# Kernel optimization log

Hardware: AMD Instinct MI355X
Metric: run time of the kernel (lower is better)

Reference implementation:

```python
import jax, jax.numpy as jnp
import numpy as np

PI = 3.14159  # constant used in the torch module
N_QUBITS = 10
N_LAYERS = 4
B = 1024  # number of graphs


def _lin_init(k, fan_in, fan_out):
    k1, k2 = jax.random.split(k)
    s = 1.0 / np.sqrt(fan_in)
    W = jax.random.uniform(k1, (fan_in, fan_out), jnp.float32, -s, s)
    b = jax.random.uniform(k2, (fan_out,), jnp.float32, -s, s)
    return W, b


def setup_inputs():
    key = jax.random.key(0)
    ks = jax.random.split(key, 12)
    N, E, Fin, H, Emb = 32768, 131072, 128, 256, 128
    x = jax.random.normal(ks[0], (N, Fin), jnp.float32)
    edge_index = jax.random.randint(ks[1], (2, E), 0, N)
    batch = jnp.sort(jax.random.randint(ks[2], (N,), 0, B))
    edge_attr = jax.random.uniform(ks[3], (E, 4), dtype=jnp.float32)
    W1, b1 = _lin_init(ks[4], Fin, H)          # GCNConv 1
    W2, b2 = _lin_init(ks[5], H, Emb)          # GCNConv 2
    projW, projb = _lin_init(ks[6], Emb, N_QUBITS)
    vqc_weights = jax.random.uniform(ks[7], (N_LAYERS, N_QUBITS), jnp.float32, 0.0, 2 * np.pi)
    epW, epb = _lin_init(ks[8], 4, N_QUBITS - 1)
    cW1, cb1 = _lin_init(ks[9], Emb + N_QUBITS, 16)
    cW2, cb2 = _lin_init(ks[10], 16, 1)
    return dict(x=x, edge_index=edge_index, batch=batch, edge_attr=edge_attr,
                W1=W1, b1=b1, W2=W2, b2=b2, projW=projW, projb=projb,
                vqc_weights=vqc_weights, epW=epW, epb=epb,
                cW1=cW1, cb1=cb1, cW2=cW2, cb2=cb2)


def _gcn_conv(x, W, b, src, dst, n):
    # GCNConv with self-loops: sym-normalized aggregation of xW
    h = x @ W
    deg = jnp.zeros((n,), x.dtype).at[dst].add(1.0) + 1.0  # +1 self-loop
    dinv = jax.lax.rsqrt(deg)
    coef = (dinv[src] * dinv[dst])[:, None]
    agg = jnp.zeros_like(h).at[dst].add(h[src] * coef)
    return agg + h * (1.0 / deg)[:, None] + b


def _segment_mean(v, seg, n):
    tot = jnp.zeros((n, v.shape[1]), v.dtype).at[seg].add(v)
    cnt = jnp.zeros((n,), v.dtype).at[seg].add(1.0)
    return tot / jnp.clip(cnt, 1.0)[:, None]


def _run_vqc(q_in, weights, ep):
    # Batched real state-vector simulation. All gates (RY, CRY) are real.
    # Wire 0 = most significant bit (pennylane default.qubit convention).
    b = q_in.shape[0]
    dim = 2 ** N_QUBITS
    st = jnp.zeros((b, dim), q_in.dtype).at[:, 0].set(1.0)

    def ry(st, theta, w):
        th = jnp.broadcast_to(theta, (b,)) * 0.5
        c = jnp.cos(th)[:, None, None]
        s = jnp.sin(th)[:, None, None]
        r = st.reshape(b, 2 ** w, 2, -1)
        a0, a1 = r[:, :, 0], r[:, :, 1]
        return jnp.stack([c * a0 - s * a1, s * a0 + c * a1], axis=2).reshape(b, dim)

    def cry(st, theta, w):
        # control w, target w+1 (adjacent wires)
        th = jnp.broadcast_to(theta, (b,)) * 0.5
        c = jnp.cos(th)[:, None, None]
        s = jnp.sin(th)[:, None, None]
        r = st.reshape(b, 2 ** w, 2, 2, -1)
        a0, a1 = r[:, :, 1, 0], r[:, :, 1, 1]
        r = r.at[:, :, 1, 0].set(c * a0 - s * a1).at[:, :, 1, 1].set(s * a0 + c * a1)
        return r.reshape(b, dim)

    for i in range(N_QUBITS):                      # AngleEmbedding (RY)
        st = ry(st, q_in[:, i], i)
    for layer in range(N_LAYERS):
        for i in range(N_QUBITS):
            st = ry(st, weights[layer, i], i)
        for i in range(N_QUBITS - 1):
            st = cry(st, ep[:, i], i)

    probs = st * st
    zs = []
    for i in range(N_QUBITS):
        p = probs.reshape(b, 2 ** i, 2, -1).sum(axis=(1, 3))
        zs.append(p[:, 0] - p[:, 1])               # <PauliZ(i)>
    return jnp.stack(zs, axis=1)                   # [B, n_qubits]


def reference(x, edge_index, batch, edge_attr, W1, b1, W2, b2, projW, projb,
              vqc_weights, epW, epb, cW1, cb1, cW2, cb2):
    N = x.shape[0]
    src, dst = edge_index[0], edge_index[1]
    # GCN encoder: two GCNConv + ReLU, global mean pool (dropout = eval mode)
    h = jax.nn.relu(_gcn_conv(x, W1, b1, src, dst, N))
    h = jax.nn.relu(_gcn_conv(h, W2, b2, src, dst, N))
    emb = _segment_mean(h, batch, B)               # [B, gcn_embed]

    q_in = jnp.tanh(emb @ projW + projb) * PI      # [B, n_qubits]

    # scatter-mean edge pooling per graph, then edge projection
    edge_batch = batch[src]
    pooled_edge = _segment_mean(edge_attr, edge_batch, B)  # [B, 4]
    ep = pooled_edge @ epW + epb                   # [B, n_qubits-1]

    q_out = _run_vqc(q_in, vqc_weights, ep)        # [B, n_qubits]

    combined = jnp.concatenate([emb, q_out], axis=-1)
    hid = jax.nn.relu(combined @ cW1 + cb1)
    return hid @ cW2 + cb2                         # [B, num_tasks]
```

## Files before the change

### kernel.cpp

```cpp
#include <hip/hip_runtime.h>

#define PI_F 3.14159f
#define NQ 10

__global__ void k_zero(float4* __restrict__ p, int n4) {
  int i = blockIdx.x * blockDim.x + threadIdx.x;
  int stride = gridDim.x * blockDim.x;
  float4 z = {0.f, 0.f, 0.f, 0.f};
  for (; i < n4; i += stride) p[i] = z;
}

__global__ void k_edge_setup(const int* __restrict__ dstA, const int* __restrict__ srcA,
                             const float* __restrict__ eattr, int E,
                             int* __restrict__ cnt, float* __restrict__ nsum4,
                             float* __restrict__ necnt) {
  int e = blockIdx.x * blockDim.x + threadIdx.x;
  if (e >= E) return;
  atomicAdd(&cnt[dstA[e]], 1);
  int s = srcA[e];
  float4 v = *(const float4*)(eattr + (size_t)e * 4);
  atomicAdd(&nsum4[(size_t)s * 4 + 0], v.x);
  atomicAdd(&nsum4[(size_t)s * 4 + 1], v.y);
  atomicAdd(&nsum4[(size_t)s * 4 + 2], v.z);
  atomicAdd(&nsum4[(size_t)s * 4 + 3], v.w);
  atomicAdd(&necnt[s], 1.0f);
}

__global__ __launch_bounds__(1024) void k_scan1(const int* __restrict__ cnt,
                                                int* __restrict__ incl,
                                                int* __restrict__ bsum) {
  __shared__ int buf[1024];
  int t = threadIdx.x;
  int base = blockIdx.x << 10;
  buf[t] = cnt[base + t];
  __syncthreads();
#pragma unroll
  for (int off = 1; off < 1024; off <<= 1) {
    int x = (t >= off) ? buf[t - off] : 0;
    __syncthreads();
    buf[t] += x;
    __syncthreads();
  }
  incl[base + t] = buf[t];
  if (t == 1023) bsum[blockIdx.x] = buf[t];
}

__global__ void k_node_setup(const int* __restrict__ cnt, const int* __restrict__ incl,
                             const int* __restrict__ bsum, const int* __restrict__ batch,
                             int N, int Bn, int* __restrict__ rowStart,
                             int* __restrict__ pos, float* __restrict__ dinv,
                             float* __restrict__ invdeg, int* __restrict__ starts) {
  int i = blockIdx.x * blockDim.x + threadIdx.x;
  if (i >= N) return;
  int blk = i >> 10;
  int pre = 0;
  for (int j = 0; j < blk; j++) pre += bsum[j];
  int c = cnt[i];
  int inc = incl[i] + pre;
  rowStart[i + 1] = inc;
  pos[i] = inc - c;
  if (i == 0) rowStart[0] = 0;
  float d = (float)c + 1.0f;
  dinv[i] = 1.0f / sqrtf(d);
  invdeg[i] = 1.0f / d;
  int b = batch[i];
  int bp = (i == 0) ? -1 : batch[i - 1];
  for (int g = bp + 1; g <= b; g++) starts[g] = i;
  if (i == N - 1) {
    for (int g = b + 1; g <= Bn; g++) starts[g] = N;
  }
}

__global__ void k_fill(const int* __restrict__ dst, const int* __restrict__ srcA,
                       const float* __restrict__ dinv, int E, int* __restrict__ pos,
                       int* __restrict__ srcSorted, float* __restrict__ dcoef) {
  int e = blockIdx.x * blockDim.x + threadIdx.x;
  if (e >= E) return;
  int s = srcA[e];
  int slot = atomicAdd(&pos[dst[e]], 1);
  srcSorted[slot] = s;
  dcoef[slot] = dinv[s];
}

__global__ __launch_bounds__(256) void k_gemm(const float* __restrict__ A,
                                              const float* __restrict__ B,
                                              float* __restrict__ C,
                                              int M, int K, int N) {
  __shared__ float As[64][36];
  __shared__ float Bs[32][68];
  int t = threadIdx.x;
  int tx = t & 15, ty = t >> 4;
  int row0 = blockIdx.y * 64, col0 = blockIdx.x * 64;
  float acc[4][4] = {};
  for (int k0 = 0; k0 < K; k0 += 32) {
#pragma unroll
    for (int rep = 0; rep < 2; rep++) {
      int slot = t + rep * 256;
      int r = slot >> 3;
      int cg = (slot & 7) << 2;
      float4 v = *(const float4*)(A + (size_t)(row0 + r) * K + (k0 + cg));
      *(float4*)&As[r][cg] = v;
      int r2 = slot >> 4;
      int cg2 = (slot & 15) << 2;
      float4 w = *(const float4*)(B + (size_t)(k0 + r2) * N + (col0 + cg2));
      *(float4*)&Bs[r2][cg2] = w;
    }
    __syncthreads();
#pragma unroll
    for (int kk = 0; kk < 32; kk++) {
      float av[4];
      av[0] = As[ty * 4 + 0][kk];
      av[1] = As[ty * 4 + 1][kk];
      av[2] = As[ty * 4 + 2][kk];
      av[3] = As[ty * 4 + 3][kk];
      float4 b4 = *(const float4*)&Bs[kk][tx << 2];
      float bv[4] = {b4.x, b4.y, b4.z, b4.w};
#pragma unroll
      for (int i = 0; i < 4; i++)
#pragma unroll
        for (int j = 0; j < 4; j++) acc[i][j] = fmaf(av[i], bv[j], acc[i][j]);
    }
    __syncthreads();
  }
#pragma unroll
  for (int i = 0; i < 4; i++) {
    float4 v = {acc[i][0], acc[i][1], acc[i][2], acc[i][3]};
    *(float4*)(C + (size_t)(row0 + ty * 4 + i) * N + (col0 + (tx << 2))) = v;
  }
}

__global__ __launch_bounds__(256) void k_gcn_combine(
    const float* __restrict__ hlin, const int* __restrict__ srcSorted,
    const float* __restrict__ dcoef, const int* __restrict__ rowStart,
    const float* __restrict__ dinv, const float* __restrict__ invdeg,
    const float* __restrict__ bias, float* __restrict__ hout, int N, int C, int shift) {
  int gid = blockIdx.x * blockDim.x + threadIdx.x;
  int n = gid >> shift;
  if (n >= N) return;
  int cq = (gid & ((1 << shift) - 1)) << 2;
  int e0 = rowStart[n], e1 = rowStart[n + 1];
  float di = dinv[n];
  float ax = 0.f, ay = 0.f, az = 0.f, aw = 0.f;
  for (int e = e0; e < e1; e++) {
    int s = srcSorted[e];
    float coef = dcoef[e] * di;
    float4 v = *(const float4*)(hlin + (size_t)s * C + cq);
    ax = fmaf(coef, v.x, ax);
    ay = fmaf(coef, v.y, ay);
    az = fmaf(coef, v.z, az);
    aw = fmaf(coef, v.w, aw);
  }
  float idg = invdeg[n];
  float4 hv = *(const float4*)(hlin + (size_t)n * C + cq);
  float4 bv = *(const float4*)(bias + cq);
  float4 r;
  r.x = fmaxf(fmaf(hv.x, idg, ax) + bv.x, 0.f);
  r.y = fmaxf(fmaf(hv.y, idg, ay) + bv.y, 0.f);
  r.z = fmaxf(fmaf(hv.z, idg, az) + bv.z, 0.f);
  r.w = fmaxf(fmaf(hv.w, idg, aw) + bv.w, 0.f);
  *(float4*)(hout + (size_t)n * C + cq) = r;
}

__device__ __forceinline__ void apply_ry(float* st, int w, float c, float s, int t) {
  int str = 1 << (9 - w);
#pragma unroll
  for (int r = 0; r < 2; r++) {
    int p = t + 256 * r;
    int lo = p & (str - 1);
    int hi = p >> (9 - w);
    int a0 = (hi << (10 - w)) + lo;
    int a1 = a0 + str;
    float x0 = st[a0], x1 = st[a1];
    st[a0] = c * x0 - s * x1;
    st[a1] = s * x0 + c * x1;
  }
}

__device__ __forceinline__ void apply_cry(float* st, int w, float c, float s, int t) {
  int ts = 1 << (8 - w);
  int lo = t & (ts - 1);
  int hi = t >> (8 - w);
  int a0 = (hi << (10 - w)) + (ts << 1) + lo;
  int a1 = a0 + ts;
  float x0 = st[a0], x1 = st[a1];
  st[a0] = c * x0 - s * x1;
  st[a1] = s * x0 + c * x1;
}

__global__ __launch_bounds__(256) void k_vqc_head(
    const float* __restrict__ h2, const int* __restrict__ starts,
    const float* __restrict__ nsum4, const float* __restrict__ necnt,
    const float* __restrict__ projW, const float* __restrict__ projb,
    const float* __restrict__ vqcW, const float* __restrict__ epW,
    const float* __restrict__ epb, const float* __restrict__ cW1,
    const float* __restrict__ cb1, const float* __restrict__ cW2,
    const float* __restrict__ cb2, float* __restrict__ out) {
  int g = blockIdx.x;
  int t = threadIdx.x;
  __shared__ float st[1024];
  __shared__ float emb[128];
  __shared__ float csc[59], css[59];
  __shared__ float pool[5];
  __shared__ float zred[4][NQ];
  __shared__ float zq[NQ];
  __shared__ float hid[16];

  int s0 = starts[g], s1 = starts[g + 1];
  int cntn = s1 - s0;
  float invc = 1.0f / (float)(cntn > 0 ? cntn : 1);
  if (t < 128) {
    float sum = 0.f;
    for (int i = s0; i < s1; i++) sum += h2[(size_t)i * 128 + t];
    emb[t] = sum * invc;
  } else if (t >= 192) {
    int lane = t - 192;
    float p0 = 0.f, p1 = 0.f, p2 = 0.f, p3 = 0.f, pc = 0.f;
    for (int i = s0 + lane; i < s1; i += 64) {
      float4 v = *(const float4*)(nsum4 + (size_t)i * 4);
      p0 += v.x; p1 += v.y; p2 += v.z; p3 += v.w;
      pc += necnt[i];
    }
#pragma unroll
    for (int off = 32; off >= 1; off >>= 1) {
      p0 += __shfl_down(p0, off, 64);
      p1 += __shfl_down(p1, off, 64);
      p2 += __shfl_down(p2, off, 64);
      p3 += __shfl_down(p3, off, 64);
      pc += __shfl_down(pc, off, 64);
    }
    if (lane == 0) { pool[0] = p0; pool[1] = p1; pool[2] = p2; pool[3] = p3; pool[4] = pc; }
  }
  st[t] = 0.f; st[t + 256] = 0.f; st[t + 512] = 0.f; st[t + 768] = 0.f;
  __syncthreads();

  if (t < NQ) {
    float sum = projb[t];
    for (int k = 0; k < 128; k++) sum = fmaf(emb[k], projW[k * NQ + t], sum);
    float th = tanhf(sum) * PI_F * 0.5f;
    csc[t] = cosf(th);
    css[t] = sinf(th);
  } else if (t < NQ + 40) {
    float th = vqcW[t - NQ] * 0.5f;
    csc[t] = cosf(th);
    css[t] = sinf(th);
  } else if (t < 59) {
    int i = t - 50;
    float icnt = 1.0f / fmaxf(pool[4], 1.0f);
    float sum = epb[i];
    for (int j = 0; j < 4; j++) sum = fmaf(pool[j] * icnt, epW[j * 9 + i], sum);
    float th = sum * 0.5f;
    csc[t] = cosf(th);
    css[t] = sinf(th);
  }
  if (t == 0) st[0] = 1.0f;
  __syncthreads();

  for (int i = 0; i < NQ; i++) {
    apply_ry(st, i, csc[i], css[i], t);
    __syncthreads();
  }
  for (int L = 0; L < 4; L++) {
    for (int i = 0; i < NQ; i++) {
      apply_ry(st, i, csc[10 + L * 10 + i], css[10 + L * 10 + i], t);
      __syncthreads();
    }
    for (int i = 0; i < NQ - 1; i++) {
      apply_cry(st, i, csc[50 + i], css[50 + i], t);
      __syncthreads();
    }
  }

  float z[NQ];
#pragma unroll
  for (int i = 0; i < NQ; i++) z[i] = 0.f;
#pragma unroll
  for (int r = 0; r < 4; r++) {
    int a = t + 256 * r;
    float p = st[a] * st[a];
#pragma unroll
    for (int i = 0; i < NQ; i++) z[i] += ((a >> (9 - i)) & 1) ? -p : p;
  }
#pragma unroll
  for (int off = 32; off >= 1; off >>= 1) {
#pragma unroll
    for (int i = 0; i < NQ; i++) z[i] += __shfl_down(z[i], off, 64);
  }
  int wave = t >> 6, lane = t & 63;
  if (lane == 0) {
#pragma unroll
    for (int i = 0; i < NQ; i++) zred[wave][i] = z[i];
  }
  __syncthreads();
  if (t < NQ) zq[t] = zred[0][t] + zred[1][t] + zred[2][t] + zred[3][t];
  __syncthreads();

  if (t < 16) {
    float sum = cb1[t];
    for (int k = 0; k < 128; k++) sum = fmaf(emb[k], cW1[k * 16 + t], sum);
    for (int k = 0; k < NQ; k++) sum = fmaf(zq[k], cW1[(128 + k) * 16 + t], sum);
    hid[t] = fmaxf(sum, 0.f);
  }
  __syncthreads();
  if (t == 0) {
    float sum = cb2[0];
    for (int j = 0; j < 16; j++) sum = fmaf(hid[j], cW2[j], sum);
    out[g] = sum;
  }
}

extern "C" void kernel_launch(void* const* d_in, const int* in_sizes, int n_in,
                              void* d_out, int out_size, void* d_ws, size_t ws_size,
                              hipStream_t stream) {
  const float* x = (const float*)d_in[0];
  const int* ei = (const int*)d_in[1];
  const int* batch = (const int*)d_in[2];
  const float* eattr = (const float*)d_in[3];
  const float* W1 = (const float*)d_in[4];
  const float* b1 = (const float*)d_in[5];
  const float* W2 = (const float*)d_in[6];
  const float* b2 = (const float*)d_in[7];
  const float* projW = (const float*)d_in[8];
  const float* projb = (const float*)d_in[9];
  const float* vqcW = (const float*)d_in[10];
  const float* epW = (const float*)d_in[11];
  const float* epb = (const float*)d_in[12];
  const float* cW1 = (const float*)d_in[13];
  const float* cb1 = (const float*)d_in[14];
  const float* cW2 = (const float*)d_in[15];
  const float* cb2 = (const float*)d_in[16];
  float* out = (float*)d_out;

  const int N = in_sizes[0] / 128;
  const int E = in_sizes[1] / 2;
  const int Bn = out_size;

  const int* srcA = ei;
  const int* dstA = ei + E;

  char* ws = (char*)d_ws;
  float* bufA = (float*)ws;
  float* bufB = (float*)(ws + ((size_t)32 << 20));
  size_t off = (size_t)64 << 20;
  auto alloc = [&](size_t bytes) {
    size_t o = off;
    off += (bytes + 255) & ~(size_t)255;
    return o;
  };
  int* cnt = (int*)(ws + alloc((size_t)N * 4));
  float* nsum4 = (float*)(ws + alloc((size_t)N * 16));
  float* necnt = (float*)(ws + alloc((size_t)N * 4));
  size_t zeroEnd = off;
  int* rowStart = (int*)(ws + alloc((size_t)(N + 1) * 4));
  int* pos = (int*)(ws + alloc((size_t)N * 4));
  int* srcSorted = (int*)(ws + alloc((size_t)E * 4));
  float* dcoef = (float*)(ws + alloc((size_t)E * 4));
  float* dinv = (float*)(ws + alloc((size_t)N * 4));
  float* invdeg = (float*)(ws + alloc((size_t)N * 4));
  int* starts = (int*)(ws + alloc((size_t)(Bn + 1) * 4));
  int* incl = (int*)(ws + alloc((size_t)N * 4));
  int* bsum = (int*)(ws + alloc(64 * 4));

  int eblocks = (E + 255) / 256;
  int nblocks = (N + 255) / 256;
  int nb1024 = N >> 10;

  int zero4 = (int)((zeroEnd - ((size_t)64 << 20)) / 16);
  k_zero<<<(zero4 + 255) / 256, 256, 0, stream>>>((float4*)(ws + ((size_t)64 << 20)), zero4);

  k_edge_setup<<<eblocks, 256, 0, stream>>>(dstA, srcA, eattr, E, cnt, nsum4, necnt);
  k_scan1<<<nb1024, 1024, 0, stream>>>(cnt, incl, bsum);
  k_node_setup<<<nblocks, 256, 0, stream>>>(cnt, incl, bsum, batch, N, Bn, rowStart, pos,
                                            dinv, invdeg, starts);
  k_fill<<<eblocks, 256, 0, stream>>>(dstA, srcA, dinv, E, pos, srcSorted, dcoef);

  {
    dim3 grid(256 / 64, N / 64);
    k_gemm<<<grid, 256, 0, stream>>>(x, W1, bufA, N, 128, 256);
  }
  k_gcn_combine<<<(N * 64) / 256, 256, 0, stream>>>(bufA, srcSorted, dcoef, rowStart,
                                                    dinv, invdeg, b1, bufB, N, 256, 6);
  {
    dim3 grid(128 / 64, N / 64);
    k_gemm<<<grid, 256, 0, stream>>>(bufB, W2, bufA, N, 256, 128);
  }
  k_gcn_combine<<<(N * 32) / 256, 256, 0, stream>>>(bufA, srcSorted, dcoef, rowStart,
                                                    dinv, invdeg, b2, bufB, N, 128, 5);
  k_vqc_head<<<Bn, 256, 0, stream>>>(bufB, starts, nsum4, necnt, projW, projb, vqcW, epW,
                                     epb, cW1, cb1, cW2, cb2, out);
}
```

Baseline: 208.8 us.

## Pool edge attributes per graph in LDS bins instead of per-node global atomics

```diff
diff --git a/kernel.cpp b/kernel.cpp
--- a/kernel.cpp
+++ b/kernel.cpp
@@ -2,6 +2,7 @@
 
 #define PI_F 3.14159f
 #define NQ 10
+#define PB 64
 
 __global__ void k_zero(float4* __restrict__ p, int n4) {
   int i = blockIdx.x * blockDim.x + threadIdx.x;
@@ -10,20 +11,35 @@
   for (; i < n4; i += stride) p[i] = z;
 }
 
-__global__ void k_edge_setup(const int* __restrict__ dstA, const int* __restrict__ srcA,
-                             const float* __restrict__ eattr, int E,
-                             int* __restrict__ cnt, float* __restrict__ nsum4,
-                             float* __restrict__ necnt) {
+__global__ void k_count(const int* __restrict__ dstA, int E, int* __restrict__ cnt) {
   int e = blockIdx.x * blockDim.x + threadIdx.x;
-  if (e >= E) return;
-  atomicAdd(&cnt[dstA[e]], 1);
-  int s = srcA[e];
-  float4 v = *(const float4*)(eattr + (size_t)e * 4);
-  atomicAdd(&nsum4[(size_t)s * 4 + 0], v.x);
-  atomicAdd(&nsum4[(size_t)s * 4 + 1], v.y);
-  atomicAdd(&nsum4[(size_t)s * 4 + 2], v.z);
-  atomicAdd(&nsum4[(size_t)s * 4 + 3], v.w);
-  atomicAdd(&necnt[s], 1.0f);
+  if (e < E) atomicAdd(&cnt[dstA[e]], 1);
+}
+
+__global__ __launch_bounds__(1024) void k_edge_pool(const int* __restrict__ srcA,
+                                                    const int* __restrict__ batch,
+                                                    const float* __restrict__ eattr, int E,
+                                                    float* __restrict__ part) {
+  __shared__ float bins[1024 * 5];
+  int t = threadIdx.x;
+  for (int i = t; i < 5120; i += 1024) bins[i] = 0.f;
+  __syncthreads();
+  int per = (E + gridDim.x - 1) / gridDim.x;
+  int base = blockIdx.x * per;
+  int end = min(base + per, E);
+  for (int e = base + t; e < end; e += 1024) {
+    int s = srcA[e];
+    int g = batch[s];
+    float4 v = *(const float4*)(eattr + (size_t)e * 4);
+    atomicAdd(&bins[g * 5 + 0], v.x);
+    atomicAdd(&bins[g * 5 + 1], v.y);
+    atomicAdd(&bins[g * 5 + 2], v.z);
+    atomicAdd(&bins[g * 5 + 3], v.w);
+    atomicAdd(&bins[g * 5 + 4], 1.0f);
+  }
+  __syncthreads();
+  float* dst = part + (size_t)blockIdx.x * 5120;
+  for (int i = t; i < 5120; i += 1024) dst[i] = bins[i];
 }
 
 __global__ __launch_bounds__(1024) void k_scan1(const int* __restrict__ cnt,
@@ -189,12 +205,12 @@
 
 __global__ __launch_bounds__(256) void k_vqc_head(
     const float* __restrict__ h2, const int* __restrict__ starts,
-    const float* __restrict__ nsum4, const float* __restrict__ necnt,
-    const float* __restrict__ projW, const float* __restrict__ projb,
-    const float* __restrict__ vqcW, const float* __restrict__ epW,
-    const float* __restrict__ epb, const float* __restrict__ cW1,
-    const float* __restrict__ cb1, const float* __restrict__ cW2,
-    const float* __restrict__ cb2, float* __restrict__ out) {
+    const float* __restrict__ part, const float* __restrict__ projW,
+    const float* __restrict__ projb, const float* __restrict__ vqcW,
+    const float* __restrict__ epW, const float* __restrict__ epb,
+    const float* __restrict__ cW1, const float* __restrict__ cb1,
+    const float* __restrict__ cW2, const float* __restrict__ cb2,
+    float* __restrict__ out) {
   int g = blockIdx.x;
   int t = threadIdx.x;
   __shared__ float st[1024];
@@ -215,10 +231,9 @@
   } else if (t >= 192) {
     int lane = t - 192;
     float p0 = 0.f, p1 = 0.f, p2 = 0.f, p3 = 0.f, pc = 0.f;
-    for (int i = s0 + lane; i < s1; i += 64) {
-      float4 v = *(const float4*)(nsum4 + (size_t)i * 4);
-      p0 += v.x; p1 += v.y; p2 += v.z; p3 += v.w;
-      pc += necnt[i];
+    for (int b = lane; b < PB; b += 64) {
+      const float* pp = part + (size_t)b * 5120 + g * 5;
+      p0 += pp[0]; p1 += pp[1]; p2 += pp[2]; p3 += pp[3]; pc += pp[4];
     }
 #pragma unroll
     for (int off = 32; off >= 1; off >>= 1) {
@@ -347,9 +362,8 @@
     return o;
   };
   int* cnt = (int*)(ws + alloc((size_t)N * 4));
-  float* nsum4 = (float*)(ws + alloc((size_t)N * 16));
-  float* necnt = (float*)(ws + alloc((size_t)N * 4));
   size_t zeroEnd = off;
+  float* part = (float*)(ws + alloc((size_t)PB * 5120 * 4));
   int* rowStart = (int*)(ws + alloc((size_t)(N + 1) * 4));
   int* pos = (int*)(ws + alloc((size_t)N * 4));
   int* srcSorted = (int*)(ws + alloc((size_t)E * 4));
@@ -367,7 +381,8 @@
   int zero4 = (int)((zeroEnd - ((size_t)64 << 20)) / 16);
   k_zero<<<(zero4 + 255) / 256, 256, 0, stream>>>((float4*)(ws + ((size_t)64 << 20)), zero4);
 
-  k_edge_setup<<<eblocks, 256, 0, stream>>>(dstA, srcA, eattr, E, cnt, nsum4, necnt);
+  k_count<<<eblocks, 256, 0, stream>>>(dstA, E, cnt);
+  k_edge_pool<<<PB, 1024, 0, stream>>>(srcA, batch, eattr, E, part);
   k_scan1<<<nb1024, 1024, 0, stream>>>(cnt, incl, bsum);
   k_node_setup<<<nblocks, 256, 0, stream>>>(cnt, incl, bsum, batch, N, Bn, rowStart, pos,
                                             dinv, invdeg, starts);
@@ -385,6 +400,6 @@
   }
   k_gcn_combine<<<(N * 32) / 256, 256, 0, stream>>>(bufA, srcSorted, dcoef, rowStart,
                                                     dinv, invdeg, b2, bufB, N, 128, 5);
-  k_vqc_head<<<Bn, 256, 0, stream>>>(bufB, starts, nsum4, necnt, projW, projb, vqcW, epW,
+  k_vqc_head<<<Bn, 256, 0, stream>>>(bufB, starts, part, projW, projb, vqcW, epW,
                                      epb, cW1, cb1, cW2, cb2, out);
 }
```

Result: faster. 193.4 us (-7.4%).
